# Optimization experiments

Measured on AMD Instinct MI355X. Metric: run time of the kernel, lower is better.

Reference implementation:

```python
import jax, jax.numpy as jnp
import numpy as np

N = 50000
E = 800000
D_IN = 128
H = 128
K = 64
BN_EPS = 1e-5


def setup_inputs() -> dict:
    key = jax.random.key(0)
    ks = jax.random.split(key, 16)
    s_in = 1.0 / np.sqrt(D_IN)
    s_h = 1.0 / np.sqrt(H)
    inp = {
        "x": jax.random.normal(ks[0], (N, D_IN), dtype=jnp.float32),
        "edge_index": jax.random.randint(ks[1], (2, E), 0, N, dtype=jnp.int64),
        # GIN layer 1 MLP (Linear(D_IN,H) -> ReLU -> Linear(H,H)), eps1, BN1
        "W1a": jax.random.uniform(ks[2], (D_IN, H), jnp.float32, -s_in, s_in),
        "b1a": jnp.zeros((H,), jnp.float32),
        "W1b": jax.random.uniform(ks[3], (H, H), jnp.float32, -s_h, s_h),
        "b1b": jnp.zeros((H,), jnp.float32),
        "eps1": jnp.zeros((), jnp.float32),
        "gamma1": jnp.ones((H,), jnp.float32),
        "beta1": jnp.zeros((H,), jnp.float32),
        # GIN layer 2 MLP, eps2, BN2
        "W2a": jax.random.uniform(ks[4], (H, H), jnp.float32, -s_h, s_h),
        "b2a": jnp.zeros((H,), jnp.float32),
        "W2b": jax.random.uniform(ks[5], (H, H), jnp.float32, -s_h, s_h),
        "b2b": jnp.zeros((H,), jnp.float32),
        "eps2": jnp.zeros((), jnp.float32),
        "gamma2": jnp.ones((H,), jnp.float32),
        "beta2": jnp.zeros((H,), jnp.float32),
        # final projection (no bias) and learnable log temperature
        "Wout": jax.random.uniform(ks[6], (H, K), jnp.float32, -s_h, s_h),
        "log_tau": jnp.zeros((), jnp.float32),  # log(1.0)
    }
    return inp


def _gin_layer(x, src, dst, Wa, ba, Wb, bb, eps):
    # GINConv: mlp((1+eps)*x + sum_{j in N(i)} x_j), scatter-add over edges
    agg = jax.ops.segment_sum(x[src], dst, num_segments=N)  # [N, d]
    h = (1.0 + eps) * x + agg
    h = jax.nn.relu(h @ Wa + ba) @ Wb + bb
    return h


def _batchnorm(x, gamma, beta):
    # training-mode BatchNorm1d over node dim (biased variance)
    m = jnp.mean(x, axis=0)
    v = jnp.mean(jnp.square(x - m), axis=0)
    return (x - m) * jax.lax.rsqrt(v + BN_EPS) * gamma + beta


def reference(x, edge_index, W1a, b1a, W1b, b1b, eps1, gamma1, beta1,
              W2a, b2a, W2b, b2b, eps2, gamma2, beta2, Wout, log_tau):
    src, dst = edge_index[0], edge_index[1]
    h = _gin_layer(x, src, dst, W1a, b1a, W1b, b1b, eps1)
    h = jax.nn.relu(_batchnorm(h, gamma1, beta1))
    h = _gin_layer(h, src, dst, W2a, b2a, W2b, b2b, eps2)
    h = jax.nn.relu(_batchnorm(h, gamma2, beta2))
    logits = h @ Wout  # [N, K]
    tau = jnp.exp(log_tau)
    S = jax.nn.softmax(logits / tau, axis=-1)
    return (S, logits)
```

## Files before the change

kernel.cpp:

```cpp
#include <hip/hip_runtime.h>
#include <hip/hip_fp16.h>


#define NNODES 50000
#define NEDGES 800000
#define HD 128
#define KOUT 64
#define NCLS 8
#define CLSW 6250
#define HIST_BLKS 512

typedef __attribute__((ext_vector_type(8))) _Float16 f16x8;
typedef __attribute__((ext_vector_type(4))) float f32x4;

__device__ __forceinline__ unsigned short f2h_bits(float f) {
    _Float16 h = (_Float16)f;
    return __builtin_bit_cast(unsigned short, h);
}
__device__ __forceinline__ f16x8 h8_relu(f16x8 v) {
    #pragma unroll
    for (int i = 0; i < 8; ++i) v[i] = (v[i] > (_Float16)0.f) ? v[i] : (_Float16)0.f;
    return v;
}
__device__ __forceinline__ void bn_fold_ch(
    const float* __restrict__ ssum, const float* __restrict__ ssq,
    const float* __restrict__ gamma, const float* __restrict__ beta,
    int c, float* sc_out, float* sh_out)
{
    float s = 0.f, q = 0.f;
    #pragma unroll
    for (int g = 0; g < 8; ++g) {
        s += ssum[g * 128 + c];
        q += ssq[g * 128 + c];
    }
    const float invN = 1.0f / (float)NNODES;
    float m = s * invN;
    float var = fmaf(-m, m, q * invN);
    float rs = rsqrtf(var + 1e-5f);
    float sc = gamma[c] * rs;
    *sc_out = sc;
    *sh_out = fmaf(-m, sc, beta[c]);
}

__global__ __launch_bounds__(256) void prep_all(
    const float* __restrict__ x, unsigned short* __restrict__ xh,
    const float* __restrict__ W1a, const float* __restrict__ W1b,
    const float* __restrict__ W2a, const float* __restrict__ W2b,
    unsigned short* __restrict__ wt1a, unsigned short* __restrict__ wt1b,
    unsigned short* __restrict__ wt2a, unsigned short* __restrict__ wt2b,
    const int* __restrict__ ei, int* __restrict__ deg)
{
    __shared__ int h[CLSW];
    int bid = blockIdx.x;
    if (bid < HIST_BLKS) {
        const int cls = bid & 7;
        const int lo = cls * CLSW;
        const int e0 = (bid >> 3) * 12500;
        for (int i = threadIdx.x; i < CLSW; i += 256) h[i] = 0;
        __syncthreads();
        for (int e = e0 + threadIdx.x; e < e0 + 12500; e += 256) {
            unsigned d = (unsigned)(ei[NEDGES + e] - lo);
            if (d < (unsigned)CLSW) atomicAdd(&h[d], 1);
        }
        __syncthreads();
        for (int i = threadIdx.x; i < CLSW; i += 256) {
            int v = h[i];
            if (v) atomicAdd(&deg[lo + i], v);
        }
    } else if (bid < HIST_BLKS + 6250) {
        int i = (bid - HIST_BLKS) * 256 + threadIdx.x;
        float4 v = ((const float4*)x)[i];
        ushort4 o;
        o.x = f2h_bits(v.x); o.y = f2h_bits(v.y);
        o.z = f2h_bits(v.z); o.w = f2h_bits(v.w);
        ((ushort4*)xh)[i] = o;
    } else {
        int wb = bid - (HIST_BLKS + 6250);
        int w = wb >> 6;
        int idx = (wb & 63) * 256 + threadIdx.x;
        int n = idx >> 7, k = idx & 127;
        const float* W = (w == 0) ? W1a : (w == 1) ? W1b : (w == 2) ? W2a : W2b;
        unsigned short* Wt = (w == 0) ? wt1a : (w == 1) ? wt1b : (w == 2) ? wt2a : wt2b;
        Wt[idx] = f2h_bits(W[k * HD + n]);
    }
}

__global__ __launch_bounds__(256) void scan_a(
    const int* __restrict__ deg, int* __restrict__ incl, int* __restrict__ bsum)
{
    __shared__ int s[256];
    int t = threadIdx.x, idx = blockIdx.x * 256 + t;
    int v = (idx < NNODES) ? deg[idx] : 0;
    s[t] = v; __syncthreads();
    #pragma unroll
    for (int off = 1; off < 256; off <<= 1) {
        int tmp = (t >= off) ? s[t - off] : 0;
        __syncthreads();
        s[t] += tmp;
        __syncthreads();
    }
    if (idx < NNODES) incl[idx] = s[t];
    if (t == 255) bsum[blockIdx.x] = s[255];
}

__global__ __launch_bounds__(256) void scan_c(
    const int* __restrict__ deg, const int* __restrict__ incl,
    const int* __restrict__ bsum,
    int* __restrict__ row_start, int* __restrict__ cur)
{
    __shared__ int s[256];
    int b = blockIdx.x, t = threadIdx.x;
    int p = 0;
    for (int i = t; i < b; i += 256) p += bsum[i];
    s[t] = p; __syncthreads();
    #pragma unroll
    for (int off = 128; off > 0; off >>= 1) {
        if (t < off) s[t] += s[t + off];
        __syncthreads();
    }
    int off0 = s[0];
    int idx = b * 256 + t;
    if (idx >= NNODES) return;
    int ex = incl[idx] - deg[idx] + off0;
    row_start[idx] = ex;
    cur[idx] = ex;
}

__global__ __launch_bounds__(256) void edge_fill(
    const int* __restrict__ ei, int* __restrict__ cur, int* __restrict__ col)
{
    const int cls = blockIdx.x & 7;
    const int e0 = (blockIdx.x >> 3) * 3125;
    for (int e = e0 + threadIdx.x; e < e0 + 3125; e += 256) {
        int dst = ei[NEDGES + e];
        if (dst / CLSW == cls) {
            int pos = atomicAdd(&cur[dst], 1);
            col[pos] = ei[e];
        }
    }
}

template<bool BN>
__global__ __launch_bounds__(256) void gin_gather_w(
    const unsigned short* __restrict__ Xh, const int* __restrict__ col,
    const int* __restrict__ rs, const int* __restrict__ re,
    const float* __restrict__ eps,
    const float* __restrict__ ssum, const float* __restrict__ ssq,
    const float* __restrict__ gamma, const float* __restrict__ beta,
    unsigned short* __restrict__ H0h)
{
    __shared__ float s_sc[128], s_sh[128];
    const int t = threadIdx.x;
    const int g = t >> 4;
    const int lane = t & 15;
    const f16x8* X8 = (const f16x8*)Xh;
    const float alphaf = 1.f + eps[0];

    if (BN) {
        if (t < 128) bn_fold_ch(ssum, ssq, gamma, beta, t, &s_sc[t], &s_sh[t]);
        __syncthreads();
    }

    f16x8 sc8, sh8, al8;
    #pragma unroll
    for (int i = 0; i < 8; ++i) al8[i] = (_Float16)alphaf;
    if (BN) {
        #pragma unroll
        for (int i = 0; i < 8; ++i) {
            sc8[i] = (_Float16)s_sc[lane * 8 + i];
            sh8[i] = (_Float16)s_sh[lane * 8 + i];
        }
    }

    #pragma unroll 1
    for (int nn = 0; nn < 2; ++nn) {
        int node = blockIdx.x * 32 + nn * 16 + g;
        if (node >= NNODES) continue;

        f16x8 acc = X8[(long)node * 16 + lane];
        if (BN) acc = h8_relu(acc * sc8 + sh8);
        acc = acc * al8;

        int j = rs[node], end = re[node];
        for (; j + 7 < end; j += 8) {
            int c0 = col[j],     c1 = col[j + 1], c2 = col[j + 2], c3 = col[j + 3];
            int c4 = col[j + 4], c5 = col[j + 5], c6 = col[j + 6], c7 = col[j + 7];
            f16x8 u0 = X8[(long)c0 * 16 + lane];
            f16x8 u1 = X8[(long)c1 * 16 + lane];
            f16x8 u2 = X8[(long)c2 * 16 + lane];
            f16x8 u3 = X8[(long)c3 * 16 + lane];
            f16x8 u4 = X8[(long)c4 * 16 + lane];
            f16x8 u5 = X8[(long)c5 * 16 + lane];
            f16x8 u6 = X8[(long)c6 * 16 + lane];
            f16x8 u7 = X8[(long)c7 * 16 + lane];
            if (BN) {
                u0 = h8_relu(u0 * sc8 + sh8); u1 = h8_relu(u1 * sc8 + sh8);
                u2 = h8_relu(u2 * sc8 + sh8); u3 = h8_relu(u3 * sc8 + sh8);
                u4 = h8_relu(u4 * sc8 + sh8); u5 = h8_relu(u5 * sc8 + sh8);
                u6 = h8_relu(u6 * sc8 + sh8); u7 = h8_relu(u7 * sc8 + sh8);
            }
            acc += ((u0 + u1) + (u2 + u3)) + ((u4 + u5) + (u6 + u7));
        }
        for (; j + 3 < end; j += 4) {
            f16x8 u0 = X8[(long)col[j]     * 16 + lane];
            f16x8 u1 = X8[(long)col[j + 1] * 16 + lane];
            f16x8 u2 = X8[(long)col[j + 2] * 16 + lane];
            f16x8 u3 = X8[(long)col[j + 3] * 16 + lane];
            if (BN) {
                u0 = h8_relu(u0 * sc8 + sh8); u1 = h8_relu(u1 * sc8 + sh8);
                u2 = h8_relu(u2 * sc8 + sh8); u3 = h8_relu(u3 * sc8 + sh8);
            }
            acc += (u0 + u1) + (u2 + u3);
        }
        for (; j < end; ++j) {
            f16x8 u = X8[(long)col[j] * 16 + lane];
            if (BN) u = h8_relu(u * sc8 + sh8);
            acc += u;
        }

        ((f16x8*)H0h)[(long)node * 16 + lane] = acc;
    }
}

__global__ __launch_bounds__(512) void mlp_mfma(
    const unsigned short* __restrict__ A,
    const unsigned short* __restrict__ Wta,
    const float* __restrict__ biasa,
    const unsigned short* __restrict__ Wtb,
    const float* __restrict__ biasb,
    unsigned short* __restrict__ Cb,
    float* __restrict__ out_sum, float* __restrict__ out_sq)
{
    __shared__ float4 smem4[69632 / 16];
    char* smem = (char*)smem4;
    _Float16 (*Wsa)[136]  = (_Float16(*)[136])smem;
    _Float16 (*Wsb)[136]  = (_Float16(*)[136])(smem + 34816);
    _Float16 (*Cs16)[136] = (_Float16(*)[136])smem;
    float (*CsF)[132]     = (float(*)[132])smem;
    float* redp           = (float*)smem;

    const int t = threadIdx.x;
    const int wave = t >> 6, lane = t & 63;
    const int m16 = lane & 15, quad = lane >> 4;
    const int row0 = blockIdx.x * 128;
    const int arow = row0 + wave * 16 + m16;

    #pragma unroll
    for (int i = 0; i < 4; ++i) {
        int idx = t + i * 512;
        int r = idx >> 4, s = idx & 15;
        *(float4*)&Wsa[r][s * 8] = ((const float4*)Wta)[idx];
        *(float4*)&Wsb[r][s * 8] = ((const float4*)Wtb)[idx];
    }

    f16x8 afrag[4];
    if (arow < NNODES) {
        const _Float16* ar = (const _Float16*)A + (long)arow * HD + quad * 8;
        #pragma unroll
        for (int kc = 0; kc < 4; ++kc)
            afrag[kc] = *(const f16x8*)(ar + kc * 32);
    } else {
        #pragma unroll
        for (int kc = 0; kc < 4; ++kc)
            afrag[kc] = f16x8{0, 0, 0, 0, 0, 0, 0, 0};
    }
    __syncthreads();

    f32x4 accs[8];
    #pragma unroll
    for (int np = 0; np < 8; np += 2) {
        f32x4 a0 = {0.f, 0.f, 0.f, 0.f};
        f32x4 a1 = {0.f, 0.f, 0.f, 0.f};
        const _Float16* b0 = &Wsa[np * 16 + m16][quad * 8];
        const _Float16* b1 = &Wsa[(np + 1) * 16 + m16][quad * 8];
        #pragma unroll
        for (int kc = 0; kc < 4; ++kc) {
            f16x8 f0 = *(const f16x8*)(b0 + kc * 32);
            f16x8 f1 = *(const f16x8*)(b1 + kc * 32);
            a0 = __builtin_amdgcn_mfma_f32_16x16x32_f16(afrag[kc], f0, a0, 0, 0, 0);
            a1 = __builtin_amdgcn_mfma_f32_16x16x32_f16(afrag[kc], f1, a1, 0, 0, 0);
        }
        accs[np] = a0; accs[np + 1] = a1;
    }
    __syncthreads();

    #pragma unroll
    for (int np = 0; np < 8; ++np) {
        int c = np * 16 + m16;
        float bb = biasa[c];
        #pragma unroll
        for (int r = 0; r < 4; ++r)
            Cs16[wave * 16 + quad * 4 + r][c] =
                (_Float16)fmaxf(accs[np][r] + bb, 0.f);
    }
    __syncthreads();

    f16x8 afrag2[4];
    {
        const int crow = wave * 16 + m16;
        #pragma unroll
        for (int kc = 0; kc < 4; ++kc)
            afrag2[kc] = *(const f16x8*)&Cs16[crow][quad * 8 + kc * 32];
    }
    #pragma unroll
    for (int np = 0; np < 8; np += 2) {
        f32x4 a0 = {0.f, 0.f, 0.f, 0.f};
        f32x4 a1 = {0.f, 0.f, 0.f, 0.f};
        const _Float16* b0 = &Wsb[np * 16 + m16][quad * 8];
        const _Float16* b1 = &Wsb[(np + 1) * 16 + m16][quad * 8];
        #pragma unroll
        for (int kc = 0; kc < 4; ++kc) {
            f16x8 f0 = *(const f16x8*)(b0 + kc * 32);
            f16x8 f1 = *(const f16x8*)(b1 + kc * 32);
            a0 = __builtin_amdgcn_mfma_f32_16x16x32_f16(afrag2[kc], f0, a0, 0, 0, 0);
            a1 = __builtin_amdgcn_mfma_f32_16x16x32_f16(afrag2[kc], f1, a1, 0, 0, 0);
        }
        accs[np] = a0; accs[np + 1] = a1;
    }
    __syncthreads();

    #pragma unroll
    for (int np = 0; np < 8; ++np) {
        int c = np * 16 + m16;
        float bb = biasb[c];
        #pragma unroll
        for (int r = 0; r < 4; ++r)
            CsF[wave * 16 + quad * 4 + r][c] = accs[np][r] + bb;
    }
    __syncthreads();

    const int s4 = t & 31;
    const int rb = t >> 5;
    float lsum[4] = {}, lsq[4] = {};
    #pragma unroll
    for (int i = 0; i < 8; ++i) {
        int r = rb + i * 16;
        int row = row0 + r;
        float4 v = *(const float4*)&CsF[r][s4 * 4];
        if (row < NNODES) {
            ushort4 o;
            o.x = f2h_bits(v.x); o.y = f2h_bits(v.y);
            o.z = f2h_bits(v.z); o.w = f2h_bits(v.w);
            ((ushort4*)Cb)[(long)row * 32 + s4] = o;
            lsum[0] += v.x; lsum[1] += v.y; lsum[2] += v.z; lsum[3] += v.w;
            lsq[0] = fmaf(v.x, v.x, lsq[0]);
            lsq[1] = fmaf(v.y, v.y, lsq[1]);
            lsq[2] = fmaf(v.z, v.z, lsq[2]);
            lsq[3] = fmaf(v.w, v.w, lsq[3]);
        }
    }
    __syncthreads();

    #pragma unroll
    for (int j = 0; j < 4; ++j) {
        redp[(0 * 16 + rb) * 128 + s4 * 4 + j] = lsum[j];
        redp[(1 * 16 + rb) * 128 + s4 * 4 + j] = lsq[j];
    }
    __syncthreads();
    if (t < 128) {
        float s = 0.f, q = 0.f;
        #pragma unroll
        for (int g = 0; g < 16; ++g) {
            s += redp[g * 128 + t];
            q += redp[(16 + g) * 128 + t];
        }
        const int cls = blockIdx.x & 7;
        atomicAdd(&out_sum[cls * 128 + t], s);
        atomicAdd(&out_sq[cls * 128 + t],  q);
    }
}

__global__ __launch_bounds__(256) void out_proj_softmax(
    const unsigned short* __restrict__ Hh, const float* __restrict__ Wout,
    const float* __restrict__ ssum, const float* __restrict__ ssq,
    const float* __restrict__ gamma, const float* __restrict__ beta,
    const float* __restrict__ log_tau,
    float* __restrict__ outS, float* __restrict__ outL)
{
    __shared__ float As[HD][20];
    __shared__ float s_sc[128], s_sh[128];
    const int t = threadIdx.x;
    const long row0 = (long)blockIdx.x * 16;

    if (t < 128) bn_fold_ch(ssum, ssq, gamma, beta, t, &s_sc[t], &s_sh[t]);
    __syncthreads();

    {
        int r = t >> 4;
        int c0 = (t & 15) * 8;
        f16x8 v8 = *(const f16x8*)(Hh + (row0 + r) * HD + c0);
        #pragma unroll
        for (int i = 0; i < 8; ++i) {
            int cc = c0 + i;
            As[cc][r] = fmaxf(fmaf((float)v8[i], s_sc[cc], s_sh[cc]), 0.f);
        }
    }
    __syncthreads();

    const int c = t & 63;
    const int g = t >> 6;
    float acc[4] = {};

    float wq[8];
    #pragma unroll
    for (int i = 0; i < 8; ++i) wq[i] = Wout[i * KOUT + c];

    #pragma unroll 1
    for (int kc = 0; kc < HD; kc += 8) {
        float wn[8];
        if (kc + 8 < HD) {
            #pragma unroll
            for (int i = 0; i < 8; ++i) wn[i] = Wout[(kc + 8 + i) * KOUT + c];
        }
        #pragma unroll
        for (int i = 0; i < 8; ++i) {
            float4 a = *(const float4*)&As[kc + i][g * 4];
            acc[0] = fmaf(a.x, wq[i], acc[0]);
            acc[1] = fmaf(a.y, wq[i], acc[1]);
            acc[2] = fmaf(a.z, wq[i], acc[2]);
            acc[3] = fmaf(a.w, wq[i], acc[3]);
        }
        if (kc + 8 < HD) {
            #pragma unroll
            for (int i = 0; i < 8; ++i) wq[i] = wn[i];
        }
    }

    float inv_tau = __expf(-log_tau[0]);
    #pragma unroll
    for (int i = 0; i < 4; ++i) {
        float z = acc[i] * inv_tau;
        float m = z;
        #pragma unroll
        for (int o = 32; o > 0; o >>= 1) m = fmaxf(m, __shfl_xor(m, o));
        float e = __expf(z - m);
        float s = e;
        #pragma unroll
        for (int o = 32; o > 0; o >>= 1) s += __shfl_xor(s, o);
        long oi = (row0 + g * 4 + i) * KOUT + c;
        outS[oi] = e / s;
        outL[oi] = acc[i];
    }
}

extern "C" void kernel_launch(void* const* d_in, const int* in_sizes, int n_in,
                              void* d_out, int out_size, void* d_ws, size_t ws_size,
                              hipStream_t stream)
{
    const float* x      = (const float*)d_in[0];
    const int*   ei     = (const int*)d_in[1];
    const float* W1a    = (const float*)d_in[2];
    const float* b1a    = (const float*)d_in[3];
    const float* W1b    = (const float*)d_in[4];
    const float* b1b    = (const float*)d_in[5];
    const float* eps1   = (const float*)d_in[6];
    const float* gamma1 = (const float*)d_in[7];
    const float* beta1  = (const float*)d_in[8];
    const float* W2a    = (const float*)d_in[9];
    const float* b2a    = (const float*)d_in[10];
    const float* W2b    = (const float*)d_in[11];
    const float* b2b    = (const float*)d_in[12];
    const float* eps2   = (const float*)d_in[13];
    const float* gamma2 = (const float*)d_in[14];
    const float* beta2  = (const float*)d_in[15];
    const float* Wout   = (const float*)d_in[16];
    const float* ltau   = (const float*)d_in[17];

    const size_t NB = (size_t)NNODES * HD;
    float* B0 = (float*)d_ws;
    float* B1 = B0 + NB;
    float* B2 = B1 + NB;
    float* ST = B2 + NB;
    float* sum1 = ST, *sq1 = ST + 1024, *sum2 = ST + 2048, *sq2 = ST + 3072;

    unsigned short* xh  = (unsigned short*)B2;
    unsigned short* h0h = (unsigned short*)B0;
    unsigned short* hh  = (unsigned short*)B0;
    unsigned short* h2h = (unsigned short*)B2;
    unsigned short* B1h = (unsigned short*)B1;

    int* I0        = (int*)(ST + 4096);
    int* deg       = I0;
    int* incl      = I0 + 50048;
    int* row_start = I0 + 2 * 50048;
    int* cur       = I0 + 3 * 50048;
    int* bsum      = I0 + 4 * 50048;
    int* col       = bsum + 256;
    unsigned short* wt1a = (unsigned short*)(col + NEDGES);
    unsigned short* wt1b = wt1a + HD * HD;
    unsigned short* wt2a = wt1b + HD * HD;
    unsigned short* wt2b = wt2a + HD * HD;

    const int SCAN_BLKS = (NNODES + 255) / 256;
    const int GEMM_BLKS = (NNODES + 127) / 128;
    const int GATH_BLKS = (NNODES + 31) / 32;

    hipMemsetAsync(ST, 0, 4096 * sizeof(float), stream);
    hipMemsetAsync(deg, 0, NNODES * sizeof(int), stream);
    prep_all<<<HIST_BLKS + 6506, 256, 0, stream>>>(x, xh, W1a, W1b, W2a, W2b,
                                                   wt1a, wt1b, wt2a, wt2b, ei, deg);
    scan_a<<<SCAN_BLKS, 256, 0, stream>>>(deg, incl, bsum);
    scan_c<<<SCAN_BLKS, 256, 0, stream>>>(deg, incl, bsum, row_start, cur);
    edge_fill<<<2048, 256, 0, stream>>>(ei, cur, col);

    gin_gather_w<false><<<GATH_BLKS, 256, 0, stream>>>(
        xh, col, row_start, cur, eps1,
        nullptr, nullptr, nullptr, nullptr, h0h);
    mlp_mfma<<<GEMM_BLKS, 512, 0, stream>>>(
        h0h, wt1a, b1a, wt1b, b1b, hh, sum1, sq1);

    gin_gather_w<true><<<GATH_BLKS, 256, 0, stream>>>(
        hh, col, row_start, cur, eps2,
        sum1, sq1, gamma1, beta1, h2h);
    mlp_mfma<<<GEMM_BLKS, 512, 0, stream>>>(
        h2h, wt2a, b2a, wt2b, b2b, B1h, sum2, sq2);

    out_proj_softmax<<<NNODES / 16, 256, 0, stream>>>(
        B1h, Wout, sum2, sq2, gamma2, beta2, ltau,
        (float*)d_out, (float*)d_out + (size_t)NNODES * KOUT);
}
```

Before: 293.7 us.

## Sort gather nodes by degree bucket to balance per-group work

Adds a degree-by-class histogram, a bucket scan and a permutation so that the gather kernels process nodes in degree-sorted order. Each 16-lane group in a block then handles nodes of similar degree, which cuts divergence and tail imbalance inside a wavefront. In exchange it adds one extra kernel launch, atomics in the scan kernels, an indirection load per node, and node accesses that are no longer contiguous. Output rows are still written per node, so the permutation does not affect correctness.

```diff
diff --git a/kernel.cpp b/kernel.cpp
--- a/kernel.cpp
+++ b/kernel.cpp
@@ -86,12 +86,19 @@
 }
 
 __global__ __launch_bounds__(256) void scan_a(
-    const int* __restrict__ deg, int* __restrict__ incl, int* __restrict__ bsum)
+    const int* __restrict__ deg, int* __restrict__ incl, int* __restrict__ bsum,
+    int* __restrict__ dbin)
 {
     __shared__ int s[256];
+    __shared__ int hbin[512];
     int t = threadIdx.x, idx = blockIdx.x * 256 + t;
+    hbin[t] = 0; hbin[t + 256] = 0;
     int v = (idx < NNODES) ? deg[idx] : 0;
     s[t] = v; __syncthreads();
+    if (idx < NNODES) {
+        int key = ((v < 63 ? v : 63) << 3) | (idx / CLSW);
+        atomicAdd(&hbin[key], 1);
+    }
     #pragma unroll
     for (int off = 1; off < 256; off <<= 1) {
         int tmp = (t >= off) ? s[t - off] : 0;
@@ -101,15 +108,39 @@
     }
     if (idx < NNODES) incl[idx] = s[t];
     if (t == 255) bsum[blockIdx.x] = s[255];
+    __syncthreads();
+    int c0 = hbin[t];       if (c0) atomicAdd(&dbin[t], c0);
+    int c1 = hbin[t + 256]; if (c1) atomicAdd(&dbin[t + 256], c1);
+}
+
+__global__ __launch_bounds__(512) void dbin_scan(
+    const int* __restrict__ dbin, int* __restrict__ dbase)
+{
+    __shared__ int s[512];
+    int t = threadIdx.x;
+    int v = dbin[t];
+    s[t] = v; __syncthreads();
+    #pragma unroll
+    for (int off = 1; off < 512; off <<= 1) {
+        int tmp = (t >= off) ? s[t - off] : 0;
+        __syncthreads();
+        s[t] += tmp;
+        __syncthreads();
+    }
+    dbase[t] = s[t] - v;
 }
 
 __global__ __launch_bounds__(256) void scan_c(
     const int* __restrict__ deg, const int* __restrict__ incl,
-    const int* __restrict__ bsum,
-    int* __restrict__ row_start, int* __restrict__ cur)
+    const int* __restrict__ bsum, const int* __restrict__ dbase,
+    int* __restrict__ dcur,
+    int* __restrict__ row_start, int* __restrict__ cur, int* __restrict__ perm)
 {
     __shared__ int s[256];
+    __shared__ int lcount[512];
+    __shared__ int lbase[512];
     int b = blockIdx.x, t = threadIdx.x;
+    lcount[t] = 0; lcount[t + 256] = 0;
     int p = 0;
     for (int i = t; i < b; i += 256) p += bsum[i];
     s[t] = p; __syncthreads();
@@ -120,10 +151,23 @@
     }
     int off0 = s[0];
     int idx = b * 256 + t;
-    if (idx >= NNODES) return;
-    int ex = incl[idx] - deg[idx] + off0;
-    row_start[idx] = ex;
-    cur[idx] = ex;
+    bool ok = idx < NNODES;
+    int key = 0, r = 0;
+    if (ok) {
+        int dv = deg[idx];
+        int ex = incl[idx] - dv + off0;
+        row_start[idx] = ex;
+        cur[idx] = ex;
+        key = ((dv < 63 ? dv : 63) << 3) | (idx / CLSW);
+        r = atomicAdd(&lcount[key], 1);
+    }
+    __syncthreads();
+    int c0 = lcount[t];
+    lbase[t] = c0 ? atomicAdd(&dcur[t], c0) : 0;
+    int c1 = lcount[t + 256];
+    lbase[t + 256] = c1 ? atomicAdd(&dcur[t + 256], c1) : 0;
+    __syncthreads();
+    if (ok) perm[dbase[key] + lbase[key] + r] = idx;
 }
 
 __global__ __launch_bounds__(256) void edge_fill(
@@ -144,6 +188,7 @@
 __global__ __launch_bounds__(256) void gin_gather_w(
     const unsigned short* __restrict__ Xh, const int* __restrict__ col,
     const int* __restrict__ rs, const int* __restrict__ re,
+    const int* __restrict__ perm,
     const float* __restrict__ eps,
     const float* __restrict__ ssum, const float* __restrict__ ssq,
     const float* __restrict__ gamma, const float* __restrict__ beta,
@@ -174,8 +219,9 @@
 
     #pragma unroll 1
     for (int nn = 0; nn < 2; ++nn) {
-        int node = blockIdx.x * 32 + nn * 16 + g;
-        if (node >= NNODES) continue;
+        int slot = blockIdx.x * 32 + nn * 16 + g;
+        if (slot >= NNODES) continue;
+        int node = perm[slot];
 
         f16x8 acc = X8[(long)node * 16 + lane];
         if (BN) acc = h8_relu(acc * sc8 + sh8);
@@ -484,8 +530,12 @@
     int* incl      = I0 + 50048;
     int* row_start = I0 + 2 * 50048;
     int* cur       = I0 + 3 * 50048;
-    int* bsum      = I0 + 4 * 50048;
-    int* col       = bsum + 256;
+    int* perm      = I0 + 4 * 50048;
+    int* bsum      = I0 + 5 * 50048;
+    int* dbin      = bsum + 256;
+    int* dbase     = dbin + 512;
+    int* dcur      = dbase + 512;
+    int* col       = dcur + 512;
     unsigned short* wt1a = (unsigned short*)(col + NEDGES);
     unsigned short* wt1b = wt1a + HD * HD;
     unsigned short* wt2a = wt1b + HD * HD;
@@ -497,20 +547,23 @@
 
     hipMemsetAsync(ST, 0, 4096 * sizeof(float), stream);
     hipMemsetAsync(deg, 0, NNODES * sizeof(int), stream);
+    hipMemsetAsync(dbin, 0, 1536 * sizeof(int), stream);
     prep_all<<<HIST_BLKS + 6506, 256, 0, stream>>>(x, xh, W1a, W1b, W2a, W2b,
                                                    wt1a, wt1b, wt2a, wt2b, ei, deg);
-    scan_a<<<SCAN_BLKS, 256, 0, stream>>>(deg, incl, bsum);
-    scan_c<<<SCAN_BLKS, 256, 0, stream>>>(deg, incl, bsum, row_start, cur);
+    scan_a<<<SCAN_BLKS, 256, 0, stream>>>(deg, incl, bsum, dbin);
+    dbin_scan<<<1, 512, 0, stream>>>(dbin, dbase);
+    scan_c<<<SCAN_BLKS, 256, 0, stream>>>(deg, incl, bsum, dbase, dcur,
+                                          row_start, cur, perm);
     edge_fill<<<2048, 256, 0, stream>>>(ei, cur, col);
 
     gin_gather_w<false><<<GATH_BLKS, 256, 0, stream>>>(
-        xh, col, row_start, cur, eps1,
+        xh, col, row_start, cur, perm, eps1,
         nullptr, nullptr, nullptr, nullptr, h0h);
     mlp_mfma<<<GEMM_BLKS, 512, 0, stream>>>(
         h0h, wt1a, b1a, wt1b, b1b, hh, sum1, sq1);
 
     gin_gather_w<true><<<GATH_BLKS, 256, 0, stream>>>(
-        hh, col, row_start, cur, eps2,
+        hh, col, row_start, cur, perm, eps2,
         sum1, sq1, gamma1, beta1, h2h);
     mlp_mfma<<<GEMM_BLKS, 512, 0, stream>>>(
         h2h, wt2a, b2a, wt2b, b2b, B1h, sum2, sq2);
```

Measured after the change: 309.5 us. +5.4%, slower.
